# Performance work log

Measured on AMD Instinct MI355X. Metric: run time of the kernel, lower is better.

## Reference

```python
import jax, jax.numpy as jnp
from jax import lax
import numpy as np

KS = 8        # window size
SS = 4        # shift size = KS // 2
HEADS = 4


def _l2n(t, axis):
    # torch F.normalize: x / clamp(||x||_2, min=eps)
    return t / jnp.maximum(jnp.linalg.norm(t, axis=axis, keepdims=True), 1e-12)


def _to_windows(t, heads, ks):
    # 'b (head c) (h kh) (w kw) -> b head (h w) (kh kw) c'
    b, hc, H, W = t.shape
    c = hc // heads
    hW, wW = H // ks, W // ks
    t = t.reshape(b, heads, c, hW, ks, wW, ks)
    t = t.transpose(0, 1, 3, 5, 4, 6, 2)  # b,h,hW,wW,kh,kw,c
    return t.reshape(b, heads, hW * wW, ks * ks, c)


def _from_windows(t, hW, wW, ks):
    # 'b head (h w) (kh kw) c -> b (head c) (h kh) (w kw)'
    b, heads, nW, kk, c = t.shape
    t = t.reshape(b, heads, hW, wW, ks, ks, c)
    t = t.transpose(0, 1, 6, 2, 4, 3, 5)  # b,h,c,hW,kh,wW,kw
    return t.reshape(b, heads * c, hW * ks, wW * ks)


def _talk_conv(attn, w, hW, wW):
    # Conv3d(heads->heads, kernel (3,3,1), padding same) over the (hW, wW, K)
    # grid; kernel size 1 on K means an independent 2D conv per K slot, so we
    # fold K into the batch dim and run a single 2D conv.
    b, heads, nW, a1, a2 = attn.shape
    K = a1 * a2
    t = attn.reshape(b, heads, hW, wW, K).transpose(0, 4, 1, 2, 3)
    t = t.reshape(b * K, heads, hW, wW)
    t = lax.conv_general_dilated(t, w, (1, 1), 'SAME',
                                 dimension_numbers=('NCHW', 'OIHW', 'NCHW'))
    t = t.reshape(b, K, heads, hW, wW).transpose(0, 2, 3, 4, 1)
    return t.reshape(b, heads, nW, a1, a2)


def _shift_mask(H, W, ks, ss):
    # Swin-style shifted-window mask; pure numpy constant (shapes are static).
    img = np.zeros((H, W), np.float32)
    cnt = 0
    for hs in (slice(0, -ks), slice(-ks, -ss), slice(-ss, None)):
        for ws in (slice(0, -ks), slice(-ks, -ss), slice(-ss, None)):
            img[hs, ws] = cnt
            cnt += 1
    win = img.reshape(H // ks, ks, W // ks, ks).transpose(0, 2, 1, 3).reshape(-1, ks * ks)
    diff = win[:, None, :] - win[:, :, None]
    return jnp.asarray(np.where(diff != 0, -100.0, 0.0).astype(np.float32))


def _forward(x, w_quz, w_kv, temperature, r_talking, g_talking,
             b_talking_w, l_talking_w, dw_u_w, project_w, project_out_w,
             sca_w, sca_b):
    b, c, H, W = x.shape
    hW, wW = H // KS, W // KS
    quz = jnp.einsum('oc,bchw->bohw', w_quz, x)
    q, u, z = jnp.split(quz, 3, axis=1)
    kv = jnp.einsum('oc,bchw->bohw', w_kv, x)
    k, v = jnp.split(kv, 2, axis=1)
    # shift = True
    q, k, v = (jnp.roll(t, (-SS, -SS), axis=(-1, -2)) for t in (q, k, v))
    q, k, v = (_to_windows(t, HEADS, KS) for t in (q, k, v))  # b,h,nW,kk,c
    qb, ql, qg, qr = jnp.split(q, 4, axis=-1)
    kb, kl, kg, kr = jnp.split(k, 4, axis=-1)
    vb, vl, vg, vr = jnp.split(v, 4, axis=-1)
    qb, kb = _l2n(qb, -1), _l2n(kb, -1)
    ql, kl = _l2n(ql, -2), _l2n(kl, -2)
    qg, kg = _l2n(qg, -3), _l2n(kg, -3)
    qr, kr = _l2n(qr, -3), _l2n(kr, -3)
    # 4 branches (n=window index, i/j=position-in-window, c/d=per-branch chan)
    attn_b = jnp.einsum('bhnic,bhnjc->bhnij', qb, kb) * temperature[0]
    attn_l = jnp.einsum('bhnic,bhnid->bhncd', ql, kl) * temperature[1]
    attn_g = jnp.einsum('bhnic,bhnid->bhicd', qg, kg) * temperature[2]
    attn_r = jnp.einsum('bhnic,bhnjc->bhcij', qr, kr) * temperature[3]
    # talking heads
    attn_b = _talk_conv(attn_b, b_talking_w, hW, wW)
    attn_l = _talk_conv(attn_l, l_talking_w, hW, wW)
    attn_g = jnp.einsum('hklt,bhkcd->btlcd', g_talking, attn_g)
    attn_r = jnp.einsum('hcdt,bhcij->btdij', r_talking, attn_r)
    # shifted-window mask on the brightness branch
    attn_b = attn_b + _shift_mask(H, W, KS, SS)[None, None]
    attn_b, attn_l, attn_g, attn_r = (jax.nn.softmax(t, axis=-1)
                                      for t in (attn_b, attn_l, attn_g, attn_r))
    # outputs, all arranged to (b,h,n,i,c) before un-windowing
    out_b = jnp.einsum('bhnij,bhnjc->bhnic', attn_b, vb)
    out_l = jnp.einsum('bhncd,bhnid->bhnic', attn_l, vl)
    out_g = jnp.einsum('bhicd,bhnid->bhnic', attn_g, vg)
    out_r = jnp.einsum('bhcij,bhnjc->bhnic', attn_r, vr)
    out = jnp.concatenate([_from_windows(t, hW, wW, KS)
                           for t in (out_b, out_l, out_g, out_r)], axis=1)
    out = jnp.roll(out, (SS, SS), axis=(-1, -2))
    # simplified channel attention (global avg pool + 1x1 conv with bias)
    s = jnp.mean(out, axis=(2, 3))
    s = jnp.einsum('oc,bc->bo', sca_w, s) + sca_b
    out = jnp.einsum('oc,bchw->bohw', project_w, out * s[:, :, None, None])
    dw = lax.conv_general_dilated(u, dw_u_w, (1, 1), 'SAME',
                                  feature_group_count=u.shape[1],
                                  dimension_numbers=('NCHW', 'OIHW', 'NCHW'))
    out = out + dw
    return jnp.einsum('oc,bchw->bohw', project_out_w, out * z)


def setup_inputs() -> dict:
    key = jax.random.key(0)
    ks = jax.random.split(key, 12)
    dim, h_dim = 64, 128
    cd = h_dim // HEADS // 4
    b, H, W = 4, 192, 192
    r = lambda i, shp, s: jax.random.normal(ks[i], shp, jnp.float32) * s
    return {
        'x': jax.random.normal(ks[0], (b, dim, H, W), jnp.float32),
        'w_quz': r(1, (3 * h_dim, dim), 0.1),
        'w_kv': r(2, (2 * h_dim, dim), 0.1),
        'temperature': jnp.ones((4, HEADS, 1, 1, 1), jnp.float32),
        'r_talking': r(3, (HEADS, cd, cd, HEADS), 0.2),
        'g_talking': r(4, (HEADS, KS * KS, KS * KS, HEADS), 0.05),
        'b_talking_w': r(5, (HEADS, HEADS, 3, 3), 0.2),
        'l_talking_w': r(6, (HEADS, HEADS, 3, 3), 0.2),
        'dw_u_w': r(7, (h_dim, 1, 3, 3), 0.2),
        'project_w': r(8, (h_dim, h_dim), 0.08),
        'project_out_w': r(9, (dim, h_dim), 0.08),
        'sca_w': r(10, (h_dim, h_dim), 0.08),
        'sca_b': jnp.zeros((h_dim,), jnp.float32),
    }


def reference(x, w_quz, w_kv, temperature, r_talking, g_talking,
              b_talking_w, l_talking_w, dw_u_w, project_w, project_out_w,
              sca_w, sca_b):
    return _forward(x, w_quz, w_kv, temperature, r_talking, g_talking,
                    b_talking_w, l_talking_w, dw_u_w, project_w,
                    project_out_w, sca_w, sca_b)
```

## Files before the change

kernel.cpp:

```cpp
#include <hip/hip_runtime.h>
#include <cstdint>
#include <cstddef>

#define BB   4
#define CIN  64
#define HD   128
#define NH   4
#define CHW  32
#define CB   8
#define IMG  192
#define SSH  4
#define NWS  24
#define NWIN 576
#define KK   64
#define HWP  (IMG*IMG)

static const size_t NQK16  = (size_t)NH*NWIN*KK*16;
static const size_t NV32   = (size_t)NH*NWIN*KK*CHW;
static const size_t NGR    = (size_t)NH*KK*NWIN*CB;
static const size_t NSP    = (size_t)HD*HWP;
static const size_t NATTNB = (size_t)NH*NWIN*KK*KK;
static const size_t NATTNL = (size_t)NH*NWIN*64;
static const size_t NATTNG = (size_t)NH*KK*64;
static const size_t NATTNR = (size_t)NH*CB*KK*KK;
static const size_t NPART  = (size_t)8*NATTNR;

__device__ inline float wave_max(float v){
  #pragma unroll
  for (int s=1;s<64;s<<=1) v = fmaxf(v, __shfl_xor(v, s));
  return v;
}
__device__ inline float wave_sum(float v){
  #pragma unroll
  for (int s=1;s<64;s<<=1) v += __shfl_xor(v, s);
  return v;
}
__device__ inline float g8_max(float v){
  v = fmaxf(v, __shfl_xor(v,1)); v = fmaxf(v, __shfl_xor(v,2)); v = fmaxf(v, __shfl_xor(v,4));
  return v;
}
__device__ inline float g8_sum(float v){
  v += __shfl_xor(v,1); v += __shfl_xor(v,2); v += __shfl_xor(v,4);
  return v;
}
__device__ inline int regionc(int y){ return (y < IMG-8) ? 0 : ((y < IMG-4) ? 1 : 2); }

__device__ inline size_t widx(int h,int n,int i,int c){
  return (((size_t)h*NWIN + n)*KK + i)*CHW + c;
}
__device__ inline size_t widx16(int h,int n,int i,int c){
  return (((size_t)h*NWIN + n)*KK + i)*16 + c;
}
__device__ inline size_t gidx(int h,int i,int n,int c){
  return (((size_t)(h*KK + i))*NWIN + n)*CB + c;
}
__device__ inline size_t ridx(int h,int c,int n,int i){
  return (((size_t)(h*CB + c))*NWIN + n)*KK + i;
}

__global__ __launch_bounds__(256) void k1_proj(
    const float* __restrict__ x, const float* __restrict__ wquz, const float* __restrict__ wkv,
    float* __restrict__ qw, float* __restrict__ kw, float* __restrict__ vw,
    float* __restrict__ qg, float* __restrict__ kg,
    float* __restrict__ qr, float* __restrict__ kr,
    float* __restrict__ u, float* __restrict__ zbuf, int bsel)
{
  __shared__ float xs[64][20];
  int blk = blockIdx.x;
  int xc = blk % 12, y = blk / 12;
  int x0 = xc*16;
  int t = threadIdx.x;
  {
    int c = t >> 2, p4 = (t & 3)*4;
    float4 v = *(const float4*)&x[((size_t)(bsel*CIN+c)*IMG + y)*IMG + x0 + p4];
    *(float4*)&xs[c][p4] = v;
  }
  int py  = (y + IMG - SSH) % IMG;
  int kh  = py & 7, hwq = py >> 3;
  int wwA = ((x0 - SSH + IMG) % IMG) >> 3;
  int wwB = x0 >> 3;
  int wwC = (x0 + 8) >> 3;
  int pnA = hwq*NWS + wwA, pnB = hwq*NWS + wwB, pnC = hwq*NWS + wwC;
  int piA = kh*8 + 4, piB = kh*8, piC = kh*8;
  #define PN_(p) ((p)<4 ? pnA : ((p)<12 ? pnB : pnC))
  #define PI_(p) ((p)<4 ? (piA+(p)) : ((p)<12 ? (piB+(p)-4) : (piC+(p)-12)))
  __syncthreads();

  int o;
  if (t < 64)       o = (t>>4)*32 + (t&15);
  else if (t < 96)  o = ((t-64)>>3)*32 + 16 + (t&7);
  else if (t < 128) o = ((t-96)>>3)*32 + 24 + (t&7);
  else              o = t;

  for (int oi = 0; oi < 2; ++oi){
    const float* wr = (oi == 0) ? (wquz + (size_t)o*CIN) : (wkv + (size_t)o*CIN);
    float acc[16];
    #pragma unroll
    for (int p = 0; p < 16; ++p) acc[p] = 0.f;
    for (int cc = 0; cc < 64; cc += 4){
      float4 w4 = *(const float4*)(wr + cc);
      #pragma unroll
      for (int p = 0; p < 16; ++p){
        acc[p] += w4.x * xs[cc  ][p];
        acc[p] += w4.y * xs[cc+1][p];
        acc[p] += w4.z * xs[cc+2][p];
        acc[p] += w4.w * xs[cc+3][p];
      }
    }
    if (t < 64){
      float* dst = (oi == 0) ? qw : kw;
      int h = t >> 4, c = t & 15;
      #pragma unroll
      for (int p = 0; p < 16; ++p) dst[widx16(h,PN_(p),PI_(p),c)] = acc[p];
    } else if (t < 96){
      float* dst = (oi == 0) ? qg : kg;
      int h = (t-64) >> 3, cg = t & 7;
      #pragma unroll
      for (int p = 0; p < 16; ++p) dst[gidx(h,PI_(p),PN_(p),cg)] = acc[p];
    } else if (t < 128){
      float* dst = (oi == 0) ? qr : kr;
      int h = (t-96) >> 3, cr = t & 7;
      *(float4*)&dst[ridx(h,cr,pnA,piA)]   = make_float4(acc[0],acc[1],acc[2],acc[3]);
      *(float4*)&dst[ridx(h,cr,pnB,piB)]   = make_float4(acc[4],acc[5],acc[6],acc[7]);
      *(float4*)&dst[ridx(h,cr,pnB,piB+4)] = make_float4(acc[8],acc[9],acc[10],acc[11]);
      *(float4*)&dst[ridx(h,cr,pnC,piC)]   = make_float4(acc[12],acc[13],acc[14],acc[15]);
    } else if (oi == 0){
      size_t ub = ((size_t)(o-128)*IMG + y)*IMG + x0;
      *(float4*)&u[ub+ 0] = make_float4(acc[0],acc[1],acc[2],acc[3]);
      *(float4*)&u[ub+ 4] = make_float4(acc[4],acc[5],acc[6],acc[7]);
      *(float4*)&u[ub+ 8] = make_float4(acc[8],acc[9],acc[10],acc[11]);
      *(float4*)&u[ub+12] = make_float4(acc[12],acc[13],acc[14],acc[15]);
    } else {
      int oc = o - 128; int h = oc >> 5, c = oc & 31;
      #pragma unroll
      for (int p = 0; p < 16; ++p) vw[widx(h,PN_(p),PI_(p),c)] = acc[p];
    }
  }

  {
    int zr = t >> 1, ph = t & 1;
    const float* wr = wquz + (size_t)(256 + zr)*CIN;
    int pb = ph*8;
    float acc[8];
    #pragma unroll
    for (int p = 0; p < 8; ++p) acc[p] = 0.f;
    for (int cc = 0; cc < 64; cc += 4){
      float4 w4 = *(const float4*)(wr + cc);
      #pragma unroll
      for (int p = 0; p < 8; ++p){
        acc[p] += w4.x * xs[cc  ][pb+p];
        acc[p] += w4.y * xs[cc+1][pb+p];
        acc[p] += w4.z * xs[cc+2][pb+p];
        acc[p] += w4.w * xs[cc+3][pb+p];
      }
    }
    size_t zb = ((size_t)zr*IMG + y)*IMG + x0 + pb;
    *(float4*)&zbuf[zb]   = make_float4(acc[0],acc[1],acc[2],acc[3]);
    *(float4*)&zbuf[zb+4] = make_float4(acc[4],acc[5],acc[6],acc[7]);
  }
  #undef PN_
  #undef PI_
}

__global__ __launch_bounds__(256) void kA(
    const float* __restrict__ qw, const float* __restrict__ kw,
    const float* __restrict__ qg, const float* __restrict__ kg,
    const float* __restrict__ qr, const float* __restrict__ kr,
    const float* __restrict__ temp,
    float* __restrict__ attnB, float* __restrict__ attnL,
    float* __restrict__ attnG, float* __restrict__ part,
    float* __restrict__ invqr, float* __restrict__ invkr)
{
  __shared__ __align__(16) char smem[36864];
  int blk = blockIdx.x;
  int t = threadIdx.x;

  if (blk < 576){
    float (*qs)[64][8] = (float(*)[64][8])smem;
    int wv = t >> 6, j = t & 63;
    int gid = blk*4 + wv;
    int n = gid % NWIN, h = gid / NWIN;
    size_t base = widx16(h,n,j,0);
    float q8[CB], k8[CB];
    float sq = 0.f, sk2 = 0.f;
    #pragma unroll
    for (int c = 0; c < CB; ++c){
      q8[c] = qw[base+c]; sq += q8[c]*q8[c];
      k8[c] = kw[base+c]; sk2 += k8[c]*k8[c];
    }
    float invq = 1.f/fmaxf(sqrtf(sq),1e-12f), invk = 1.f/fmaxf(sqrtf(sk2),1e-12f);
    #pragma unroll
    for (int c = 0; c < CB; ++c){ qs[wv][j][c] = q8[c]*invq; k8[c] *= invk; }
    __syncthreads();
    float tmp = temp[h];
    float* orow = attnB + (size_t)gid*KK*KK;
    for (int i = 0; i < KK; ++i){
      float a = 0.f;
      #pragma unroll
      for (int c = 0; c < CB; ++c) a += qs[wv][i][c]*k8[c];
      orow[(size_t)i*KK + j] = a * tmp;
    }
  } else if (blk < 1152){
    int b2 = blk - 576;
    float (*qs)[64][8] = (float(*)[64][8])smem;
    float (*ks)[64][8] = (float(*)[64][8])(smem + 8192);
    float (*invqA)[8] = (float(*)[8])(smem + 16384);
    float (*invkA)[8] = (float(*)[8])(smem + 16384 + 128);
    int wv = t >> 6, tl = t & 63;
    int gid = b2*4 + wv;
    int n = gid % NWIN, h = gid / NWIN;
    size_t base = widx16(h,n,tl,8);
    #pragma unroll
    for (int c = 0; c < CB; ++c){ qs[wv][tl][c] = qw[base+c]; ks[wv][tl][c] = kw[base+c]; }
    __syncthreads();
    int c8 = tl & 7, ig = tl >> 3;
    float sq = 0.f, sk2 = 0.f;
    for (int i = ig; i < KK; i += 8){
      float a = qs[wv][i][c8]; sq += a*a;
      float b = ks[wv][i][c8]; sk2 += b*b;
    }
    #pragma unroll
    for (int m = 8; m < 64; m <<= 1){ sq += __shfl_xor(sq,m); sk2 += __shfl_xor(sk2,m); }
    if (tl < 8){ invqA[wv][tl] = 1.f/fmaxf(sqrtf(sq),1e-12f); invkA[wv][tl] = 1.f/fmaxf(sqrtf(sk2),1e-12f); }
    __syncthreads();
    int c = tl >> 3, d = tl & 7;
    float a = 0.f;
    for (int i = 0; i < KK; ++i) a += qs[wv][i][c]*ks[wv][i][d];
    attnL[(size_t)gid*64 + tl] = a * invqA[wv][c] * invkA[wv][d] * temp[NH + h];
  } else if (blk < 1408){
    int b2 = blk - 1152;
    int i = b2 & 63, h = b2 >> 6;
    float* sq = (float*)smem;
    float* sk = sq + 512;
    float (*redA)[64] = (float(*)[64])(smem + 4096);
    float (*redQ)[64] = (float(*)[64])(smem + 4096 + 1024);
    float (*redK)[64] = (float(*)[64])(smem + 4096 + 2048);
    size_t base = ((size_t)(h*KK+i))*NWIN*CB;
    int np = t >> 6, cd = t & 63, c = cd >> 3, d = cd & 7;
    float a = 0.f, qs2 = 0.f, ks2 = 0.f;
    for (int n0 = 0; n0 < NWIN; n0 += 64){
      __syncthreads();
      for (int idx = t; idx < 512; idx += 256){
        sq[idx] = qg[base + (size_t)n0*CB + idx];
        sk[idx] = kg[base + (size_t)n0*CB + idx];
      }
      __syncthreads();
      for (int nn = np; nn < 64; nn += 4){
        float qv = sq[nn*8+c], kv = sk[nn*8+d];
        a += qv*kv; qs2 += qv*qv; ks2 += kv*kv;
      }
    }
    __syncthreads();
    redA[np][cd] = a; redQ[np][cd] = qs2; redK[np][cd] = ks2;
    __syncthreads();
    if (t < 64){
      float at = redA[0][t]+redA[1][t]+redA[2][t]+redA[3][t];
      float qt = redQ[0][t]+redQ[1][t]+redQ[2][t]+redQ[3][t];
      float kt = redK[0][t]+redK[1][t]+redK[2][t]+redK[3][t];
      at *= (1.f/fmaxf(sqrtf(qt),1e-12f)) * (1.f/fmaxf(sqrtf(kt),1e-12f)) * temp[2*NH + h];
      attnG[(size_t)(h*KK+i)*64 + t] = at;
    }
  } else if (blk < 1664){
    int b2 = blk - 1408;
    int chunk = b2 >> 5, hc = b2 & 31;
    int n0 = chunk*72;
    float* sq = (float*)smem;
    float* sk = sq + 72*64;
    size_t base = (size_t)hc*NWIN*KK + (size_t)n0*KK;
    for (int idx = t; idx < 72*64/4; idx += 256){
      *(float4*)&sq[idx*4] = *(const float4*)&qr[base + (size_t)idx*4];
      *(float4*)&sk[idx*4] = *(const float4*)&kr[base + (size_t)idx*4];
    }
    __syncthreads();
    int j = t & 63, ig = t >> 6;
    float acc[16];
    #pragma unroll
    for (int p = 0; p < 16; ++p) acc[p] = 0.f;
    for (int nn = 0; nn < 72; ++nn){
      float kv = sk[nn*64+j];
      #pragma unroll
      for (int p = 0; p < 16; ++p) acc[p] += sq[nn*64 + ig*16 + p]*kv;
    }
    float* ob = part + (size_t)b2*4096;
    #pragma unroll
    for (int p = 0; p < 16; ++p) ob[(size_t)(ig*16+p)*64 + j] = acc[p];
  } else {
    int hc = blk - 1664;
    float (*rq)[64] = (float(*)[64])smem;
    float (*rk)[64] = (float(*)[64])(smem + 1024);
    size_t base = (size_t)hc*NWIN*KK;
    int i = t & 63, ng = t >> 6;
    float sq = 0.f, sk2 = 0.f;
    for (int n = ng; n < NWIN; n += 4){
      float a = qr[base + (size_t)n*KK + i]; sq  += a*a;
      float b = kr[base + (size_t)n*KK + i]; sk2 += b*b;
    }
    rq[ng][i] = sq; rk[ng][i] = sk2;
    __syncthreads();
    if (t < 64){
      float s = rq[0][t]+rq[1][t]+rq[2][t]+rq[3][t];
      invqr[hc*KK + t] = 1.f/fmaxf(sqrtf(s),1e-12f);
    } else if (t < 128){
      int i2 = t - 64;
      float s = rk[0][i2]+rk[1][i2]+rk[2][i2]+rk[3][i2];
      invkr[hc*KK + i2] = 1.f/fmaxf(sqrtf(s),1e-12f);
    }
  }
}

__global__ __launch_bounds__(256) void kB(
    const float* __restrict__ attnB, const float* __restrict__ btw,
    const float* __restrict__ vw, float* __restrict__ outa,
    const float* __restrict__ attnL, const float* __restrict__ ltw,
    const float* __restrict__ attnG, const float* __restrict__ gtalk,
    float* __restrict__ attnGp,
    const float* __restrict__ part, const float* __restrict__ invqr,
    const float* __restrict__ invkr, const float* __restrict__ temp,
    float* __restrict__ attnR,
    const float* __restrict__ u, const float* __restrict__ dww,
    float* __restrict__ dwu)
{
  __shared__ __align__(16) char smem[12800];
  int blk = blockIdx.x;
  int t = threadIdx.x;

  if (blk < 9216){
    float (*pbuf)[4][66] = (float(*)[4][66])smem;
    float (*vv)[8][66]   = (float(*)[8][66])(smem + 4224);
    int ig = blk / NWIN, n = blk % NWIN;
    int i0 = ig*4;
    int hw = n / NWS, ww = n % NWS;
    int w = t >> 6, l = t & 63;
    {
      size_t vb = widx(w, n, l, 0);
      float4 va = *(const float4*)&vw[vb];
      float4 vb4 = *(const float4*)&vw[vb + 4];
      vv[w][0][l] = va.x;  vv[w][1][l] = va.y;  vv[w][2][l] = va.z;  vv[w][3][l] = va.w;
      vv[w][4][l] = vb4.x; vv[w][5][l] = vb4.y; vv[w][6][l] = vb4.z; vv[w][7][l] = vb4.w;
    }
    int i = i0 + w;
    float a0 = 0.f, a1 = 0.f, a2 = 0.f, a3 = 0.f;
    #pragma unroll
    for (int nb = 0; nb < 9; ++nb){
      const int dy = nb/3 - 1, dx = nb%3 - 1;
      int hw2 = hw + dy, ww2 = ww + dx;
      if (hw2 >= 0 && hw2 < NWS && ww2 >= 0 && ww2 < NWS){
        int n2 = hw2*NWS + ww2;
        #pragma unroll
        for (int h = 0; h < 4; ++h){
          float r = attnB[((size_t)(h*NWIN + n2)*KK + i)*KK + l];
          a0 += btw[(0*4 + h)*9 + nb] * r;
          a1 += btw[(1*4 + h)*9 + nb] * r;
          a2 += btw[(2*4 + h)*9 + nb] * r;
          a3 += btw[(3*4 + h)*9 + nb] * r;
        }
      }
    }
    int kh = i >> 3, kwd = i & 7;
    int cntI = regionc(hw*8 + kh)*3 + regionc(ww*8 + kwd);
    int cntJ = regionc(hw*8 + (l>>3))*3 + regionc(ww*8 + (l&7));
    float mval = (cntI != cntJ) ? -100.f : 0.f;
    a0 += mval; a1 += mval; a2 += mval; a3 += mval;
    {
      float m0 = wave_max(a0); float e0 = __expf(a0 - m0); pbuf[0][w][l] = e0 / wave_sum(e0);
      float m1 = wave_max(a1); float e1 = __expf(a1 - m1); pbuf[1][w][l] = e1 / wave_sum(e1);
      float m2 = wave_max(a2); float e2 = __expf(a2 - m2); pbuf[2][w][l] = e2 / wave_sum(e2);
      float m3 = wave_max(a3); float e3 = __expf(a3 - m3); pbuf[3][w][l] = e3 / wave_sum(e3);
    }
    __syncthreads();
    {
      int i2 = l >> 4, c = (l >> 1) & 7, jq = l & 1;
      const float* pr = &pbuf[w][i2][jq*32];
      const float* vr = &vv[w][c][jq*32];
      float s = 0.f;
      #pragma unroll
      for (int q = 0; q < 32; ++q) s += pr[q] * vr[q];
      s += __shfl_xor(s, 1);
      if (jq == 0){
        int ii = i0 + i2;
        int khh = ii >> 3, kww = ii & 7;
        int Y = (hw*8 + khh + SSH) % IMG;
        int X = (ww*8 + kww + SSH) % IMG;
        outa[((size_t)(w*CB + c)*HWP) + (size_t)Y*IMG + X] = s;
      }
    }
  } else if (blk < 9792){
    int n = blk - 9216;
    int hw = n/NWS, ww = n%NWS;
    float (*rows)[9][64] = (float(*)[9][64])smem;
    float* wt = (float*)(smem + 9216);
    float (*P)[8][8] = (float(*)[8][8])(smem + 9792);
    if (t < NH*NH*9) wt[t] = ltw[t];
    for (int l = t; l < NH*9*64; l += 256){
      int h = l/(9*64); int nb = (l/64)%9; int cd = l & 63;
      int dy = nb/3-1, dx = nb%3-1; int hw2 = hw+dy, ww2 = ww+dx;
      float v = 0.f;
      if (hw2>=0 && hw2<NWS && ww2>=0 && ww2<NWS)
        v = attnL[((size_t)h*NWIN + hw2*NWS + ww2)*64 + cd];
      rows[h][nb][cd] = v;
    }
    __syncthreads();
    int tt = t >> 6; int cd = t & 63; int c = cd >> 3, d = cd & 7;
    float a = 0.f;
    #pragma unroll
    for (int h = 0; h < NH; ++h)
      #pragma unroll
      for (int nb = 0; nb < 9; ++nb)
        a += wt[(tt*NH + h)*9 + nb] * rows[h][nb][cd];
    float m = g8_max(a);
    float e = __expf(a - m);
    P[tt][c][d] = e / g8_sum(e);
    __syncthreads();
    int i = t & 63;
    size_t vbase = widx(tt, n, i, 8);
    float vl[CB];
    #pragma unroll
    for (int d2 = 0; d2 < CB; ++d2) vl[d2] = vw[vbase + d2];
    int kh = i>>3, kwd = i&7;
    int Y = (hw*8+kh+SSH)%IMG, X = (ww*8+kwd+SSH)%IMG;
    #pragma unroll
    for (int c2 = 0; c2 < CB; ++c2){
      float o = 0.f;
      #pragma unroll
      for (int d2 = 0; d2 < CB; ++d2) o += P[tt][c2][d2]*vl[d2];
      outa[((size_t)(32 + tt*CB + c2)*IMG + Y)*IMG + X] = o;
    }
  } else if (blk < 9856){
    int bb = blk - 9792;
    int w = t >> 6, cd = t & 63;
    int idx = bb*4 + w;
    int l = idx & 63, t2 = idx >> 6;
    float a = 0.f;
    for (int h = 0; h < NH; ++h)
      for (int k = 0; k < KK; ++k)
        a += gtalk[((size_t)(h*KK + k)*KK + l)*NH + t2] * attnG[((size_t)h*KK + k)*64 + cd];
    float m = g8_max(a);
    float e = __expf(a - m);
    attnGp[((size_t)t2*KK + l)*64 + cd] = e / g8_sum(e);
  } else if (blk < 10368){
    int e = (blk - 9856)*256 + t;
    float s = 0.f;
    #pragma unroll
    for (int ch = 0; ch < 8; ++ch) s += part[(size_t)ch*NATTNR + e];
    int hc = e >> 12, ij = e & 4095, i = ij >> 6, j = ij & 63;
    attnR[e] = s * invqr[hc*64+i] * invkr[hc*64+j] * temp[3*NH + (hc>>3)];
  } else {
    int bb = blk - 10368;
    int ch = bb / 48; int y0 = (bb % 48) * 4;
    float (*rows)[192] = (float(*)[192])smem;
    for (int idx = t; idx < 6*48; idx += 256){
      int r = idx / 48, px4 = (idx % 48)*4;
      int yy = y0 - 1 + r;
      float4 v = {0.f,0.f,0.f,0.f};
      if (yy >= 0 && yy < IMG) v = *(const float4*)&u[(size_t)ch*HWP + (size_t)yy*IMG + px4];
      rows[r][px4] = v.x; rows[r][px4+1] = v.y; rows[r][px4+2] = v.z; rows[r][px4+3] = v.w;
    }
    float kw9[9];
    #pragma unroll
    for (int q = 0; q < 9; ++q) kw9[q] = dww[ch*9 + q];
    __syncthreads();
    int r = t >> 6, lane = t & 63;
    for (int kx = 0; kx < 3; ++kx){
      int px = lane + kx*64;
      float s = 0.f;
      #pragma unroll
      for (int dy = 0; dy < 3; ++dy){
        #pragma unroll
        for (int dx = -1; dx <= 1; ++dx){
          int xx = px + dx;
          if (xx >= 0 && xx < IMG) s += kw9[dy*3 + dx + 1] * rows[r+dy][xx];
        }
      }
      dwu[(size_t)ch*HWP + (size_t)(y0+r)*IMG + px] = s;
    }
  }
}

__global__ __launch_bounds__(256) void kC(
    const float* __restrict__ attnGp, const float* __restrict__ vw,
    float* __restrict__ outa,
    const float* __restrict__ attnR, const float* __restrict__ rtalk,
    float* __restrict__ attnRp)
{
  __shared__ __align__(16) char smem[16512];
  int blk = blockIdx.x;
  int t = threadIdx.x;

  if (blk < 2304){
    float* P = (float*)smem;
    int n = blk % NWIN; int t2 = blk / NWIN;
    for (int l = t; l < KK*64; l += 256) P[l] = attnGp[(size_t)t2*KK*64 + l];
    __syncthreads();
    int i = t >> 2; int c0 = (t & 3)*2;
    size_t vbase = widx(t2, n, i, 16);
    float vg[8];
    #pragma unroll
    for (int d = 0; d < 8; ++d) vg[d] = vw[vbase + d];
    int hw = n/NWS, ww = n%NWS; int kh = i>>3, kwd = i&7;
    int Y = (hw*8+kh+SSH)%IMG, X = (ww*8+kwd+SSH)%IMG;
    for (int c = c0; c < c0+2; ++c){
      float o = 0.f;
      #pragma unroll
      for (int d = 0; d < 8; ++d) o += P[(i*8 + c)*8 + d]*vg[d];
      outa[((size_t)(64 + t2*CB + c)*IMG + Y)*IMG + X] = o;
    }
  } else {
    int bb = blk - 2304;
    int d = bb % CB; int t2 = bb / CB;
    float (*S)[64] = (float(*)[64])smem;
    float* wr2 = (float*)(smem + 16384);
    if (t < 32){ int h = t >> 3, c = t & 7; wr2[t] = rtalk[((size_t)(h*CB + c)*CB + d)*NH + t2]; }
    __syncthreads();
    int j = t & 63; int ig = t >> 6;
    float acc[16];
    #pragma unroll
    for (int p = 0; p < 16; ++p) acc[p] = 0.f;
    for (int hc = 0; hc < 32; ++hc){
      float w = wr2[hc];
      const float* Ar = attnR + (size_t)hc*KK*KK;
      #pragma unroll
      for (int p = 0; p < 16; ++p) acc[p] += w * Ar[(size_t)(ig*16+p)*KK + j];
    }
    #pragma unroll
    for (int p = 0; p < 16; ++p) S[ig*16+p][j] = acc[p];
    __syncthreads();
    for (int r = ig; r < 64; r += 4){
      float a = S[r][j];
      float m = wave_max(a);
      float e = __expf(a - m);
      attnRp[(((size_t)t2*CB + d)*KK + r)*KK + j] = e / wave_sum(e);
    }
  }
}

__global__ __launch_bounds__(256) void k7c(
    const float* __restrict__ attnRp, const float* __restrict__ vw, float* __restrict__ outa)
{
  int n = blockIdx.x % NWIN; int t2 = blockIdx.x / NWIN;
  __shared__ float vr[KK][CB];
  int t = threadIdx.x;
  for (int l = t; l < KK*CB; l += 256){
    int j = l >> 3, c = l & 7;
    vr[j][c] = vw[widx(t2, n, j, 24 + c)];
  }
  __syncthreads();
  int i = t & 63; int cg = t >> 6;
  int hw = n/NWS, ww = n%NWS; int kh = i>>3, kwd = i&7;
  int Y = (hw*8+kh+SSH)%IMG, X = (ww*8+kwd+SSH)%IMG;
  for (int c = cg*2; c < cg*2+2; ++c){
    const float* Pr = attnRp + (((size_t)t2*CB + c)*KK + i)*KK;
    float o = 0.f;
    for (int j = 0; j < KK; ++j) o += Pr[j]*vr[j][c];
    outa[((size_t)(96 + t2*CB + c)*IMG + Y)*IMG + X] = o;
  }
}

__global__ __launch_bounds__(256) void k8_mean(const float* __restrict__ outa, float* __restrict__ meanb){
  int ch = blockIdx.x;
  const float4* p = (const float4*)(outa + (size_t)ch*HWP);
  float s = 0.f;
  for (int l = threadIdx.x; l < HWP/4; l += 256){
    float4 v = p[l]; s += v.x+v.y+v.z+v.w;
  }
  __shared__ float red[256];
  red[threadIdx.x] = s; __syncthreads();
  for (int k = 128; k > 0; k >>= 1){
    if (threadIdx.x < k) red[threadIdx.x] += red[threadIdx.x + k];
    __syncthreads();
  }
  if (threadIdx.x == 0) meanb[ch] = red[0] / (float)HWP;
}

#define PADX 68
__global__ __launch_bounds__(256) void k9a(
    const float* __restrict__ outa, const float* __restrict__ meanb,
    const float* __restrict__ scaw, const float* __restrict__ scab,
    const float* __restrict__ projw, const float* __restrict__ dwu,
    const float* __restrict__ zbuf, float* __restrict__ out2z)
{
  __shared__ float WT[128][128];
  __shared__ float xsv[128][PADX];
  __shared__ float sv[128];
  int t = threadIdx.x;
  if (t < 128){
    float s = scab[t];
    const float* srow = scaw + (size_t)t*HD;
    for (int c = 0; c < HD; c += 4){
      float4 w = *(const float4*)&srow[c];
      float4 mm = *(const float4*)&meanb[c];
      s += w.x*mm.x + w.y*mm.y + w.z*mm.z + w.w*mm.w;
    }
    sv[t] = s;
  }
  for (int idx = t; idx < 4096; idx += 256){
    int o = idx & 127; int c4 = (idx >> 7) * 4;
    float4 w = *(const float4*)&projw[(size_t)o*HD + c4];
    WT[c4][o] = w.x; WT[c4+1][o] = w.y; WT[c4+2][o] = w.z; WT[c4+3][o] = w.w;
  }
  int px4 = (t & 15) * 4; int og8 = (t >> 4) * 8;
  for (int tile = 0; tile < 2; ++tile){
    int tid = blockIdx.x * 2 + tile;
    int y = tid / 3, x0 = (tid % 3) * 64;
    size_t sb = (size_t)y*IMG + x0;
    __syncthreads();
    for (int idx = t; idx < 2048; idx += 256){
      int c = idx >> 4; int p4 = (idx & 15) * 4;
      float4 v = *(const float4*)&outa[(size_t)c*HWP + sb + p4];
      float s = sv[c];
      xsv[c][p4] = v.x*s; xsv[c][p4+1] = v.y*s; xsv[c][p4+2] = v.z*s; xsv[c][p4+3] = v.w*s;
    }
    __syncthreads();
    float acc[8][4];
    #pragma unroll
    for (int a = 0; a < 8; ++a){ acc[a][0]=0.f; acc[a][1]=0.f; acc[a][2]=0.f; acc[a][3]=0.f; }
    for (int c = 0; c < 128; ++c){
      float4 xv = *(const float4*)&xsv[c][px4];
      float4 wA = *(const float4*)&WT[c][og8];
      float4 wB = *(const float4*)&WT[c][og8+4];
      float w8[8] = {wA.x,wA.y,wA.z,wA.w,wB.x,wB.y,wB.z,wB.w};
      #pragma unroll
      for (int a = 0; a < 8; ++a){
        acc[a][0] += w8[a]*xv.x; acc[a][1] += w8[a]*xv.y;
        acc[a][2] += w8[a]*xv.z; acc[a][3] += w8[a]*xv.w;
      }
    }
    #pragma unroll
    for (int oo = 0; oo < 8; ++oo){
      int o = og8 + oo;
      size_t off = (size_t)o*HWP + sb + px4;
      float4 d = *(const float4*)&dwu[off];
      float4 z = *(const float4*)&zbuf[off];
      float4 r;
      r.x = (acc[oo][0]+d.x)*z.x; r.y = (acc[oo][1]+d.y)*z.y;
      r.z = (acc[oo][2]+d.z)*z.z; r.w = (acc[oo][3]+d.w)*z.w;
      *(float4*)&out2z[off] = r;
    }
  }
}

__global__ __launch_bounds__(256) void k9b(
    const float* __restrict__ out2z, const float* __restrict__ projow,
    float* __restrict__ dout, int bsel)
{
  __shared__ float WT2[128][64];
  __shared__ float xsv[128][PADX];
  int t = threadIdx.x;
  for (int idx = t; idx < 2048; idx += 256){
    int o = idx & 63; int c4 = (idx >> 6) * 4;
    float4 w = *(const float4*)&projow[(size_t)o*HD + c4];
    WT2[c4][o] = w.x; WT2[c4+1][o] = w.y; WT2[c4+2][o] = w.z; WT2[c4+3][o] = w.w;
  }
  int px4 = (t & 15) * 4; int og4 = (t >> 4) * 4;
  for (int tile = 0; tile < 2; ++tile){
    int tid = blockIdx.x * 2 + tile;
    int y = tid / 3, x0 = (tid % 3) * 64;
    size_t sb = (size_t)y*IMG + x0;
    __syncthreads();
    for (int idx = t; idx < 2048; idx += 256){
      int c = idx >> 4; int p4 = (idx & 15) * 4;
      float4 v = *(const float4*)&out2z[(size_t)c*HWP + sb + p4];
      xsv[c][p4] = v.x; xsv[c][p4+1] = v.y; xsv[c][p4+2] = v.z; xsv[c][p4+3] = v.w;
    }
    __syncthreads();
    float acc[4][4];
    #pragma unroll
    for (int a = 0; a < 4; ++a){ acc[a][0]=0.f; acc[a][1]=0.f; acc[a][2]=0.f; acc[a][3]=0.f; }
    for (int c = 0; c < 128; ++c){
      float4 xv = *(const float4*)&xsv[c][px4];
      float4 w4 = *(const float4*)&WT2[c][og4];
      float w4a[4] = {w4.x,w4.y,w4.z,w4.w};
      #pragma unroll
      for (int a = 0; a < 4; ++a){
        acc[a][0] += w4a[a]*xv.x; acc[a][1] += w4a[a]*xv.y;
        acc[a][2] += w4a[a]*xv.z; acc[a][3] += w4a[a]*xv.w;
      }
    }
    #pragma unroll
    for (int oo = 0; oo < 4; ++oo){
      int o = og4 + oo;
      float4 r; r.x = acc[oo][0]; r.y = acc[oo][1]; r.z = acc[oo][2]; r.w = acc[oo][3];
      *(float4*)&dout[(size_t)(bsel*CIN + o)*HWP + sb + px4] = r;
    }
  }
}

extern "C" void kernel_launch(void* const* d_in, const int* in_sizes, int n_in,
                              void* d_out, int out_size, void* d_ws, size_t ws_size,
                              hipStream_t stream)
{
  const float* x     = (const float*)d_in[0];
  const float* wquz  = (const float*)d_in[1];
  const float* wkv   = (const float*)d_in[2];
  const float* temp  = (const float*)d_in[3];
  const float* rtalk = (const float*)d_in[4];
  const float* gtalk = (const float*)d_in[5];
  const float* btw   = (const float*)d_in[6];
  const float* ltw   = (const float*)d_in[7];
  const float* dww   = (const float*)d_in[8];
  const float* projw = (const float*)d_in[9];
  const float* projow= (const float*)d_in[10];
  const float* scaw  = (const float*)d_in[11];
  const float* scab  = (const float*)d_in[12];
  float* dout = (float*)d_out;

  float* ws = (float*)d_ws;
  float* qw    = ws;
  float* kw    = qw + NQK16;
  float* vw    = kw + NQK16;
  float* qg    = vw + NV32;
  float* kg    = qg + NGR;
  float* qr    = kg + NGR;
  float* kr    = qr + NGR;
  float* u     = kr + NGR;
  float* zbuf  = u + NSP;
  float* outa  = zbuf + NSP;
  float* attnB = outa + NSP;
  float* attnL = attnB + NATTNB;
  float* attnG = attnL + NATTNL;
  float* attnGp= attnG + NATTNG;
  float* part  = attnGp + NATTNG;
  float* attnR = part + NPART;
  float* attnRp= attnR + NATTNR;
  float* invqr = attnRp + NATTNR;
  float* invkr = invqr + 2048;
  float* meanb = invkr + 2048;
  float* dwu   = qw;
  float* out2z = attnB;

  for (int b = 0; b < BB; ++b){
    k1_proj<<<IMG*12, 256, 0, stream>>>(x, wquz, wkv, qw, kw, vw, qg, kg, qr, kr, u, zbuf, b);

    kA<<<1696, 256, 0, stream>>>(qw, kw, qg, kg, qr, kr, temp,
                                 attnB, attnL, attnG, part, invqr, invkr);

    kB<<<16512, 256, 0, stream>>>(attnB, btw, vw, outa, attnL, ltw,
                                  attnG, gtalk, attnGp, part, invqr, invkr, temp, attnR,
                                  u, dww, dwu);

    kC<<<2336, 256, 0, stream>>>(attnGp, vw, outa, attnR, rtalk, attnRp);

    k7c<<<NH*NWIN, 256, 0, stream>>>(attnRp, vw, outa);

    k8_mean<<<HD, 256, 0, stream>>>(outa, meanb);

    k9a<<<288, 256, 0, stream>>>(outa, meanb, scaw, scab, projw, dwu, zbuf, out2z);
    k9b<<<288, 256, 0, stream>>>(out2z, projow, dout, b);
  }
}
```

Measured before the change: 1.265 ms.

## Transpose u and z stores through LDS and remap kB block order

Result: no change. 1.275 ms (+0.7%).

```diff
diff --git a/kernel.cpp b/kernel.cpp
--- a/kernel.cpp
+++ b/kernel.cpp
@@ -66,6 +66,7 @@
     float* __restrict__ u, float* __restrict__ zbuf, int bsel)
 {
   __shared__ float xs[64][20];
+  __shared__ float tb[128][17];
   int blk = blockIdx.x;
   int xc = blk % 12, y = blk / 12;
   int x0 = xc*16;
@@ -92,8 +93,8 @@
   else if (t < 128) o = ((t-96)>>3)*32 + 24 + (t&7);
   else              o = t;
 
-  for (int oi = 0; oi < 2; ++oi){
-    const float* wr = (oi == 0) ? (wquz + (size_t)o*CIN) : (wkv + (size_t)o*CIN);
+  {
+    const float* wr = wquz + (size_t)o*CIN;
     float acc[16];
     #pragma unroll
     for (int p = 0; p < 16; ++p) acc[p] = 0.f;
@@ -108,28 +109,65 @@
       }
     }
     if (t < 64){
-      float* dst = (oi == 0) ? qw : kw;
       int h = t >> 4, c = t & 15;
       #pragma unroll
-      for (int p = 0; p < 16; ++p) dst[widx16(h,PN_(p),PI_(p),c)] = acc[p];
+      for (int p = 0; p < 16; ++p) qw[widx16(h,PN_(p),PI_(p),c)] = acc[p];
     } else if (t < 96){
-      float* dst = (oi == 0) ? qg : kg;
       int h = (t-64) >> 3, cg = t & 7;
       #pragma unroll
-      for (int p = 0; p < 16; ++p) dst[gidx(h,PI_(p),PN_(p),cg)] = acc[p];
+      for (int p = 0; p < 16; ++p) qg[gidx(h,PI_(p),PN_(p),cg)] = acc[p];
     } else if (t < 128){
-      float* dst = (oi == 0) ? qr : kr;
       int h = (t-96) >> 3, cr = t & 7;
-      *(float4*)&dst[ridx(h,cr,pnA,piA)]   = make_float4(acc[0],acc[1],acc[2],acc[3]);
-      *(float4*)&dst[ridx(h,cr,pnB,piB)]   = make_float4(acc[4],acc[5],acc[6],acc[7]);
-      *(float4*)&dst[ridx(h,cr,pnB,piB+4)] = make_float4(acc[8],acc[9],acc[10],acc[11]);
-      *(float4*)&dst[ridx(h,cr,pnC,piC)]   = make_float4(acc[12],acc[13],acc[14],acc[15]);
-    } else if (oi == 0){
-      size_t ub = ((size_t)(o-128)*IMG + y)*IMG + x0;
-      *(float4*)&u[ub+ 0] = make_float4(acc[0],acc[1],acc[2],acc[3]);
-      *(float4*)&u[ub+ 4] = make_float4(acc[4],acc[5],acc[6],acc[7]);
-      *(float4*)&u[ub+ 8] = make_float4(acc[8],acc[9],acc[10],acc[11]);
-      *(float4*)&u[ub+12] = make_float4(acc[12],acc[13],acc[14],acc[15]);
+      *(float4*)&qr[ridx(h,cr,pnA,piA)]   = make_float4(acc[0],acc[1],acc[2],acc[3]);
+      *(float4*)&qr[ridx(h,cr,pnB,piB)]   = make_float4(acc[4],acc[5],acc[6],acc[7]);
+      *(float4*)&qr[ridx(h,cr,pnB,piB+4)] = make_float4(acc[8],acc[9],acc[10],acc[11]);
+      *(float4*)&qr[ridx(h,cr,pnC,piC)]   = make_float4(acc[12],acc[13],acc[14],acc[15]);
+    } else {
+      int ch = o - 128;
+      #pragma unroll
+      for (int p = 0; p < 16; ++p) tb[ch][p] = acc[p];
+    }
+  }
+  __syncthreads();
+  {
+    int px = t & 15, chg = t >> 4;
+    size_t ub = (size_t)y*IMG + x0 + px;
+    #pragma unroll
+    for (int cc = 0; cc < 8; ++cc){
+      int ch = chg*8 + cc;
+      u[(size_t)ch*HWP + ub] = tb[ch][px];
+    }
+  }
+
+  {
+    const float* wr = wkv + (size_t)o*CIN;
+    float acc[16];
+    #pragma unroll
+    for (int p = 0; p < 16; ++p) acc[p] = 0.f;
+    for (int cc = 0; cc < 64; cc += 4){
+      float4 w4 = *(const float4*)(wr + cc);
+      #pragma unroll
+      for (int p = 0; p < 16; ++p){
+        acc[p] += w4.x * xs[cc  ][p];
+        acc[p] += w4.y * xs[cc+1][p];
+        acc[p] += w4.z * xs[cc+2][p];
+        acc[p] += w4.w * xs[cc+3][p];
+      }
+    }
+    if (t < 64){
+      int h = t >> 4, c = t & 15;
+      #pragma unroll
+      for (int p = 0; p < 16; ++p) kw[widx16(h,PN_(p),PI_(p),c)] = acc[p];
+    } else if (t < 96){
+      int h = (t-64) >> 3, cg = t & 7;
+      #pragma unroll
+      for (int p = 0; p < 16; ++p) kg[gidx(h,PI_(p),PN_(p),cg)] = acc[p];
+    } else if (t < 128){
+      int h = (t-96) >> 3, cr = t & 7;
+      *(float4*)&kr[ridx(h,cr,pnA,piA)]   = make_float4(acc[0],acc[1],acc[2],acc[3]);
+      *(float4*)&kr[ridx(h,cr,pnB,piB)]   = make_float4(acc[4],acc[5],acc[6],acc[7]);
+      *(float4*)&kr[ridx(h,cr,pnB,piB+4)] = make_float4(acc[8],acc[9],acc[10],acc[11]);
+      *(float4*)&kr[ridx(h,cr,pnC,piC)]   = make_float4(acc[12],acc[13],acc[14],acc[15]);
     } else {
       int oc = o - 128; int h = oc >> 5, c = oc & 31;
       #pragma unroll
@@ -137,6 +175,7 @@
     }
   }
 
+  __syncthreads();
   {
     int zr = t >> 1, ph = t & 1;
     const float* wr = wquz + (size_t)(256 + zr)*CIN;
@@ -154,9 +193,18 @@
         acc[p] += w4.w * xs[cc+3][pb+p];
       }
     }
-    size_t zb = ((size_t)zr*IMG + y)*IMG + x0 + pb;
-    *(float4*)&zbuf[zb]   = make_float4(acc[0],acc[1],acc[2],acc[3]);
-    *(float4*)&zbuf[zb+4] = make_float4(acc[4],acc[5],acc[6],acc[7]);
+    #pragma unroll
+    for (int p = 0; p < 8; ++p) tb[zr][pb+p] = acc[p];
+  }
+  __syncthreads();
+  {
+    int px = t & 15, chg = t >> 4;
+    size_t zb = (size_t)y*IMG + x0 + px;
+    #pragma unroll
+    for (int cc = 0; cc < 8; ++cc){
+      int ch = chg*8 + cc;
+      zbuf[(size_t)ch*HWP + zb] = tb[ch][px];
+    }
   }
   #undef PN_
   #undef PI_
@@ -325,9 +373,10 @@
   int t = threadIdx.x;
 
   if (blk < 9216){
+    int wk = (blk & 7)*1152 + (blk >> 3);
     float (*pbuf)[4][66] = (float(*)[4][66])smem;
     float (*vv)[8][66]   = (float(*)[8][66])(smem + 4224);
-    int ig = blk / NWIN, n = blk % NWIN;
+    int ig = wk / NWIN, n = wk % NWIN;
     int i0 = ig*4;
     int hw = n / NWS, ww = n % NWS;
     int w = t >> 6, l = t & 63;
```
